# Kernel tuning notes

Hardware: AMD Instinct MI355X
Metric: run time of the kernel (lower is better)

The kernel has to match this reference:

```python
import jax, jax.numpy as jnp
import numpy as np

HIDDEN = 4096
NH = 32          # num query heads
NKV = 8          # num kv heads
HD = HIDDEN // NH  # 128
THETA = 10000.0
L = 4096         # llama_context_len (attention-sink window)
BS = 16          # paged KV block size
B = 16           # decode batch
MAXB = 385       # blocks per sequence
NBLOCKS = B * MAXB
CTX = 6145       # context_len for every sequence (num_past = 6144)


def rope(x, pos):
    """Neox-style RoPE. x: [..., H, HD]; pos: broadcastable to x.shape[:-2]."""
    half = HD // 2
    inv_freq = 1.0 / (THETA ** (jnp.arange(half, dtype=jnp.float32) * 2.0 / HD))
    ang = pos.astype(jnp.float32)[..., None] * inv_freq      # [..., half]
    cos = jnp.cos(ang)[..., None, :]                          # [..., 1, half]
    sin = jnp.sin(ang)[..., None, :]
    x1, x2 = x[..., :half], x[..., half:]
    return jnp.concatenate([x1 * cos - x2 * sin, x2 * cos + x1 * sin], axis=-1)


def setup_inputs() -> dict:
    key = jax.random.key(0)
    ks = jax.random.split(key, 6)
    hidden_states = jax.random.normal(ks[0], (B, HIDDEN), jnp.float32)
    positions = jax.random.randint(ks[1], (B,), 0, CTX).astype(jnp.int32)
    key_cache = jax.random.normal(ks[2], (NBLOCKS, NKV, HD, BS), jnp.float32)
    value_cache = jax.random.normal(ks[3], (NBLOCKS, NKV, HD, BS), jnp.float32)
    block_tables = jnp.arange(B * MAXB, dtype=jnp.int32).reshape(B, MAXB)
    w_qkv = jax.random.normal(ks[4], (HIDDEN, (NH + 2 * NKV) * HD), jnp.float32) * 0.02
    w_o = jax.random.normal(ks[5], (NH * HD, HIDDEN), jnp.float32) * 0.02
    return {
        "positions": positions,
        "hidden_states": hidden_states,
        "key_cache": key_cache,
        "value_cache": value_cache,
        "block_tables": block_tables,
        "context_len": CTX,
        "w_qkv": w_qkv,
        "w_o": w_o,
    }


def reference(positions, hidden_states, key_cache, value_cache, block_tables,
              context_len, w_qkv, w_o):
    # ---- qkv projection + split ----
    qkv = hidden_states @ w_qkv
    q, k, v = jnp.split(qkv, [NH * HD, NH * HD + NKV * HD], axis=-1)
    # ---- clamp positions to sink window and rope current q, k ----
    clamped = jnp.minimum(positions, L - 1)
    q = rope(q.reshape(B, NH, HD), clamped)          # [B, NH, HD]
    k = rope(k.reshape(B, NKV, HD), clamped)         # [B, NKV, HD]
    v = v.reshape(B, NKV, HD)

    # ---- static sink-window geometry (context_len is a Python int) ----
    num_past = context_len - 1
    blocks_to_ignore = (num_past - L) // BS + 1
    start = num_past - L + 1 + BS
    end = num_past

    # capped block table: token t<BS -> sink block bt[0];
    # t>=BS -> bt[blocks_to_ignore + t//BS]
    t = jnp.arange(L)
    logical = jnp.where(t < BS, 0, blocks_to_ignore + t // BS)   # [L]
    offset = t % BS                                              # [L]
    abs_pos = logical * BS + offset                              # [L] absolute position in seq

    phys = block_tables[:, logical]                              # [B, L]
    K = key_cache[phys, :, :, offset]                            # [B, L, NKV, HD]
    V = value_cache[phys, :, :, offset]

    # ---- sink RoPE rewrite: keys in [start, end) get an extra rotation at abs_pos-start ----
    rot_mask = (abs_pos >= start) & (abs_pos < end)
    K = jnp.where(rot_mask[None, :, None, None], rope(K, abs_pos - start), K)

    # ---- current token's freshly-rotated k/v occupy slot abs_pos == num_past ----
    cur = (abs_pos == num_past)
    K = jnp.where(cur[None, :, None, None], k[:, None, :, :], K)
    V = jnp.where(cur[None, :, None, None], v[:, None, :, :], V)

    # ---- GQA paged-decode attention over the 4096-token capped window ----
    valid = abs_pos <= num_past                                  # [L]
    G = NH // NKV
    qg = q.reshape(B, NKV, G, HD)
    scores = jnp.einsum('bkgd,blkd->bkgl', qg, K) * (HD ** -0.5)
    scores = jnp.where(valid[None, None, None, :], scores, jnp.finfo(scores.dtype).min)
    p = jax.nn.softmax(scores, axis=-1)
    attn = jnp.einsum('bkgl,blkd->bkgd', p, V).reshape(B, NH * HD)
    return attn @ w_o


if __name__ == "__main__":
    out = reference(**setup_inputs())
    print(out.shape, out.dtype)
```

## Files before the change

kernel.cpp:

```cpp
#include <hip/hip_runtime.h>
#include <math.h>

#define B_      16
#define NH      32
#define NKV     8
#define HD      128
#define GQ      4
#define LWIN    4096
#define BS      16
#define MAXB    385
#define HIDDEN  4096
#define QKV_COLS 6144
#define TAB_N   4100
#define T_CUR   4080
#define KS      64
#define NSPLIT  64
#define NCHUNK  8
#define SCALE   0.088388347648318447f
#define LOG1E4  9.210340371976184
#define TWO_PI  6.283185307179586
#define INV_2PI 0.15915494309189535

typedef float f4v __attribute__((ext_vector_type(4)));

__global__ void k_table(float* __restrict__ ctab, float* __restrict__ stab,
                        float* __restrict__ pk, float* __restrict__ pv) {
  int idx = blockIdx.x * 256 + threadIdx.x;
  if (idx < 64 * (TAB_N / 4)) {
    int d = idx / (TAB_N / 4);
    int q = idx - d * (TAB_N / 4);
    int i0 = q * 4;
    double f = exp(-(double)d / 64.0 * LOG1E4);
    double a = (double)(i0 - 1) * f;
    double rev = a * INV_2PI;
    rev -= rint(rev);
    float r = (float)(rev * TWO_PI);
    float c = cosf(r), s = sinf(r);
    float ff = (float)f;
    float cf = cosf(ff), sf = sinf(ff);
    int base = d * TAB_N + i0;
    ctab[base] = c; stab[base] = s;
#pragma unroll
    for (int j = 1; j < 4; j++) {
      float cn = c * cf - s * sf;
      float sn = s * cf + c * sf;
      c = cn; s = sn;
      ctab[base + j] = c; stab[base + j] = s;
    }
  }
  int nz = B_ * NKV * HD * BS;
  for (int z = idx; z < nz; z += gridDim.x * 256) { pk[z] = 0.f; pv[z] = 0.f; }
}

__global__ __launch_bounds__(128, 1) void k_gemm_part(
    const float* __restrict__ X, const float* __restrict__ W,
    float* __restrict__ part, int K, int ncols) {
  int tid = threadIdx.x;
  int k0 = blockIdx.y * KS;
  int n4 = (blockIdx.x * 128 + tid) * 4;
  f4v acc[B_];
#pragma unroll
  for (int b = 0; b < B_; b++) acc[b] = (f4v){0.f, 0.f, 0.f, 0.f};
  const float* wp = W + (size_t)k0 * ncols + n4;
  const float* xp = X + k0;
#pragma unroll
  for (int batch = 0; batch < KS / 16; batch++) {
    f4v w[16];
#pragma unroll
    for (int i = 0; i < 16; i++)
      w[i] = *(const f4v*)&wp[(size_t)(batch * 16 + i) * ncols];
#pragma unroll
    for (int i = 0; i < 16; i++) {
      int kk = batch * 16 + i;
#pragma unroll
      for (int b = 0; b < B_; b++) {
        float x = xp[b * K + kk];
        acc[b][0] = fmaf(x, w[i][0], acc[b][0]);
        acc[b][1] = fmaf(x, w[i][1], acc[b][1]);
        acc[b][2] = fmaf(x, w[i][2], acc[b][2]);
        acc[b][3] = fmaf(x, w[i][3], acc[b][3]);
      }
    }
  }
  float* pp = part + (size_t)blockIdx.y * B_ * ncols + n4;
#pragma unroll
  for (int b = 0; b < B_; b++) *(f4v*)&pp[(size_t)b * ncols] = acc[b];
}

__global__ __launch_bounds__(256) void k_qkv_finish(
    const float* __restrict__ part, const int* __restrict__ positions,
    const float* __restrict__ ctab, const float* __restrict__ stab,
    float* __restrict__ qout, float* __restrict__ pk, float* __restrict__ pv) {
  int idx = blockIdx.x * 256 + threadIdx.x;
  int b = idx / 3584;
  int u = idx - b * 3584;
  if (b >= B_) return;
  if (u < 2560) {
    int h = u >> 6, j = u & 63;
    int c1 = h * 128 + j;
    int c2 = c1 + 64;
    float s1 = 0.f, s2 = 0.f;
#pragma unroll 8
    for (int ky = 0; ky < NSPLIT; ky++) {
      const float* p = part + ((size_t)ky * B_ + b) * QKV_COLS;
      s1 += p[c1];
      s2 += p[c2];
    }
    int pos = min(positions[b], LWIN - 1);
    float c = ctab[j * TAB_N + pos + 1];
    float s = stab[j * TAB_N + pos + 1];
    float o1 = s1 * c - s2 * s;
    float o2 = s2 * c + s1 * s;
    if (h < NH) {
      qout[b * HIDDEN + c1] = o1;
      qout[b * HIDDEN + c2] = o2;
    } else {
      int kv = h - NH;
      pk[((b * NKV + kv) * HD + j) * BS] = o1;
      pk[((b * NKV + kv) * HD + j + 64) * BS] = o2;
    }
  } else {
    int vi = u - 2560;
    int kv = vi >> 7, d = vi & 127;
    int col = 5120 + vi;
    float s = 0.f;
#pragma unroll 8
    for (int ky = 0; ky < NSPLIT; ky++)
      s += part[((size_t)ky * B_ + b) * QKV_COLS + col];
    pv[((b * NKV + kv) * HD + d) * BS] = s;
  }
}

__global__ __launch_bounds__(128, 1) void k_attn(
    const float* __restrict__ kc, const float* __restrict__ vc,
    const int* __restrict__ bt, const float* __restrict__ qbuf,
    const float* __restrict__ pk, const float* __restrict__ pv,
    const float* __restrict__ ctab, const float* __restrict__ stab,
    float* __restrict__ partial) {
  __shared__ __align__(16) float qT[HD][GQ];
  __shared__ __align__(16) float p_s[512][GQ];
  __shared__ float redm[2][GQ];
  __shared__ float redl[2][GQ];
  __shared__ const float* kbase[32];
  __shared__ const float* vbase[32];

  int bx = blockIdx.x;
  int b = bx & 15, kv = bx >> 4;
  int chunk = blockIdx.y;
  int tid = threadIdx.x;
  int lane = tid & 63, wave = tid >> 6;

  for (int i = tid; i < GQ * HD; i += 128) {
    int g = i >> 7, d = i & 127;
    qT[d][g] = qbuf[b * HIDDEN + (kv * GQ + g) * HD + d];
  }
  if (tid < 32) {
    int tb = chunk * 32 + tid;
    if (tb == 255) {
      kbase[tid] = pk + (size_t)(b * NKV + kv) * (HD * BS);
      vbase[tid] = pv + (size_t)(b * NKV + kv) * (HD * BS);
    } else {
      int lg = (tb == 0) ? 0 : (129 + tb);
      size_t off = ((size_t)bt[b * MAXB + lg] * NKV + kv) * (HD * BS);
      kbase[tid] = kc + off;
      vbase[tid] = vc + off;
    }
  }
  __syncthreads();

  int blk_i = lane & 15, qq = lane >> 4;
  int t0 = chunk * 512 + wave * 256 + blk_i * 16 + qq * 4;
  const float* kb = kbase[wave * 16 + blk_i] + qq * 4;
  bool rot = (t0 >= 16) && (t0 < T_CUR);
  const float* ctp = ctab + t0;
  const float* stp = stab + t0;

  float sc[GQ][4];
#pragma unroll
  for (int g = 0; g < GQ; g++)
#pragma unroll
    for (int c = 0; c < 4; c++) sc[g][c] = 0.f;

#pragma unroll
  for (int batch = 0; batch < 8; batch++) {
    f4v k1[8], k2[8], cv[8], sv[8];
#pragma unroll
    for (int i = 0; i < 8; i++) {
      int d = batch * 8 + i;
      k1[i] = *(const f4v*)(kb + d * BS);
      k2[i] = *(const f4v*)(kb + (d + 64) * BS);
      cv[i] = *(const f4v*)(ctp + d * TAB_N);
      sv[i] = *(const f4v*)(stp + d * TAB_N);
    }
#pragma unroll
    for (int i = 0; i < 8; i++) {
      int d = batch * 8 + i;
      float4 q1 = *(const float4*)&qT[d][0];
      float4 q2 = *(const float4*)&qT[d + 64][0];
      float qg1[4] = {q1.x, q1.y, q1.z, q1.w};
      float qg2[4] = {q2.x, q2.y, q2.z, q2.w};
#pragma unroll
      for (int c = 0; c < 4; c++) {
        float cc = rot ? cv[i][c] : 1.f;
        float ss = rot ? sv[i][c] : 0.f;
        float r1 = k1[i][c] * cc - k2[i][c] * ss;
        float r2 = k2[i][c] * cc + k1[i][c] * ss;
#pragma unroll
        for (int g = 0; g < GQ; g++)
          sc[g][c] = fmaf(qg1[g], r1, fmaf(qg2[g], r2, sc[g][c]));
      }
    }
  }

  float mloc[GQ];
#pragma unroll
  for (int g = 0; g < GQ; g++) {
    float m = -3e38f;
#pragma unroll
    for (int c = 0; c < 4; c++) {
      float s = (t0 + c <= T_CUR) ? sc[g][c] * SCALE : -3e38f;
      sc[g][c] = s;
      m = fmaxf(m, s);
    }
#pragma unroll
    for (int off = 1; off < 64; off <<= 1) m = fmaxf(m, __shfl_xor(m, off, 64));
    mloc[g] = m;
  }
  if (lane == 0) {
#pragma unroll
    for (int g = 0; g < GQ; g++) redm[wave][g] = mloc[g];
  }
  __syncthreads();
  float mb[GQ];
#pragma unroll
  for (int g = 0; g < GQ; g++) mb[g] = fmaxf(redm[0][g], redm[1][g]);

  float4 prc[4];
  float ls[GQ] = {0.f, 0.f, 0.f, 0.f};
#pragma unroll
  for (int c = 0; c < 4; c++) {
    float p0 = __expf(sc[0][c] - mb[0]);
    float p1 = __expf(sc[1][c] - mb[1]);
    float p2 = __expf(sc[2][c] - mb[2]);
    float p3 = __expf(sc[3][c] - mb[3]);
    ls[0] += p0; ls[1] += p1; ls[2] += p2; ls[3] += p3;
    prc[c] = make_float4(p0, p1, p2, p3);
  }
#pragma unroll
  for (int g = 0; g < GQ; g++) {
    float v = ls[g];
#pragma unroll
    for (int off = 1; off < 64; off <<= 1) v += __shfl_xor(v, off, 64);
    ls[g] = v;
  }
  if (lane == 0) {
#pragma unroll
    for (int g = 0; g < GQ; g++) redl[wave][g] = ls[g];
  }
  int trow = t0 - chunk * 512;
#pragma unroll
  for (int c = 0; c < 4; c++) *(float4*)&p_s[trow + c][0] = prc[c];
  __syncthreads();

  float acc0 = 0.f, acc1 = 0.f, acc2 = 0.f, acc3 = 0.f;
  int d_own = tid;
#pragma unroll
  for (int bt4 = 0; bt4 < 8; bt4++) {
    f4v vr[4][4];
#pragma unroll
    for (int t = 0; t < 4; t++) {
      const float* vb = vbase[bt4 * 4 + t] + d_own * BS;
      vr[t][0] = *(const f4v*)(vb);
      vr[t][1] = *(const f4v*)(vb + 4);
      vr[t][2] = *(const f4v*)(vb + 8);
      vr[t][3] = *(const f4v*)(vb + 12);
    }
#pragma unroll
    for (int t = 0; t < 4; t++) {
      const float* pp = &p_s[(bt4 * 4 + t) * 16][0];
#pragma unroll
      for (int jq = 0; jq < 4; jq++) {
#pragma unroll
        for (int j = 0; j < 4; j++) {
          float4 pj = *(const float4*)(pp + (jq * 4 + j) * GQ);
          float vv = vr[t][jq][j];
          acc0 = fmaf(pj.x, vv, acc0);
          acc1 = fmaf(pj.y, vv, acc1);
          acc2 = fmaf(pj.z, vv, acc2);
          acc3 = fmaf(pj.w, vv, acc3);
        }
      }
    }
  }

  int pid = b * NKV + kv;
  float* pw = partial + ((size_t)pid * NCHUNK + chunk) * (GQ * 130);
  pw[0 * 130 + 2 + d_own] = acc0;
  pw[1 * 130 + 2 + d_own] = acc1;
  pw[2 * 130 + 2 + d_own] = acc2;
  pw[3 * 130 + 2 + d_own] = acc3;
  if (tid == 0) {
#pragma unroll
    for (int g = 0; g < GQ; g++) {
      pw[g * 130 + 0] = mb[g];
      pw[g * 130 + 1] = redl[0][g] + redl[1][g];
    }
  }
}

__global__ __launch_bounds__(512) void k_attn_combine(
    const float* __restrict__ partial, float* __restrict__ attn) {
  int pair = blockIdx.x;
  int tid = threadIdx.x;
  int g = tid >> 7, d = tid & 127;
  const float* pb = partial + (size_t)pair * NCHUNK * (GQ * 130) + g * 130;
  float M = -3e38f;
#pragma unroll
  for (int c = 0; c < NCHUNK; c++) M = fmaxf(M, pb[c * (GQ * 130)]);
  float L = 0.f, val = 0.f;
#pragma unroll
  for (int c = 0; c < NCHUNK; c++) {
    float m = pb[c * (GQ * 130)];
    float l = pb[c * (GQ * 130) + 1];
    float a = pb[c * (GQ * 130) + 2 + d];
    float w = __expf(m - M);
    L += l * w;
    val = fmaf(a, w, val);
  }
  int b = pair >> 3, kv = pair & 7;
  attn[b * HIDDEN + (kv * GQ + g) * HD + d] = val / L;
}

__global__ __launch_bounds__(256) void k_reduce_out(
    const float* __restrict__ part, float* __restrict__ out) {
  int idx = blockIdx.x * 256 + threadIdx.x;
  int b = idx >> 12, n = idx & 4095;
  float s = 0.f;
#pragma unroll 8
  for (int ky = 0; ky < NSPLIT; ky++)
    s += part[((size_t)ky * B_ + b) * HIDDEN + n];
  out[idx] = s;
}

extern "C" void kernel_launch(void* const* d_in, const int* in_sizes, int n_in,
                              void* d_out, int out_size, void* d_ws, size_t ws_size,
                              hipStream_t stream) {
  const int*   positions = (const int*)d_in[0];
  const float* hs        = (const float*)d_in[1];
  const float* kc        = (const float*)d_in[2];
  const float* vc        = (const float*)d_in[3];
  const int*   bt        = (const int*)d_in[4];
  const float* w_qkv     = (const float*)d_in[6];
  const float* w_o       = (const float*)d_in[7];
  float* out = (float*)d_out;

  float* ws    = (float*)d_ws;
  float* ctab  = ws;
  float* stab  = ctab + 262400;
  float* pk    = stab + 262400;
  float* pv    = pk + 262144;
  float* qbuf  = pv + 262144;
  float* apart = qbuf + 65536;
  float* attn  = apart + 532480;
  float* gpart = attn + 65536;

  k_table<<<257, 256, 0, stream>>>(ctab, stab, pk, pv);
  k_gemm_part<<<dim3(QKV_COLS / 512, NSPLIT), 128, 0, stream>>>(hs, w_qkv, gpart, HIDDEN, QKV_COLS);
  k_qkv_finish<<<(B_ * 3584) / 256, 256, 0, stream>>>(gpart, positions, ctab, stab, qbuf, pk, pv);
  k_attn<<<dim3(B_ * NKV, NCHUNK), 128, 0, stream>>>(kc, vc, bt, qbuf, pk, pv, ctab, stab, apart);
  k_attn_combine<<<B_ * NKV, 512, 0, stream>>>(apart, attn);
  k_gemm_part<<<dim3(HIDDEN / 512, NSPLIT), 128, 0, stream>>>(attn, w_o, gpart, HIDDEN, HIDDEN);
  k_reduce_out<<<(B_ * HIDDEN) / 256, 256, 0, stream>>>(gpart, out);
}
```

Baseline: 216.7 us.

## Restructure QK loop for coalesced per-block K loads with cross-lane reduction

Rewrites the QK score loop so each wave processes one paged KV block at a time, with lanes splitting the head dimension. The K and RoPE table loads become contiguous across lanes, and the partial dot products are combined with xor shuffles and staged through shared memory before the softmax. This aims to replace the previously strided per-lane K reads with coalesced ones. It also changes the split configuration (KS 128, NSPLIT 32), which adds shuffle and sync overhead and changes the launch shape.

Result: slower. 252.0 us (+16.3%).

```diff
diff --git a/kernel.cpp b/kernel.cpp
--- a/kernel.cpp
+++ b/kernel.cpp
@@ -13,8 +13,8 @@
 #define QKV_COLS 6144
 #define TAB_N   4100
 #define T_CUR   4080
-#define KS      64
-#define NSPLIT  64
+#define KS      128
+#define NSPLIT  32
 #define NCHUNK  8
 #define SCALE   0.088388347648318447f
 #define LOG1E4  9.210340371976184
@@ -168,33 +168,36 @@
   }
   __syncthreads();
 
-  int blk_i = lane & 15, qq = lane >> 4;
-  int t0 = chunk * 512 + wave * 256 + blk_i * 16 + qq * 4;
-  const float* kb = kbase[wave * 16 + blk_i] + qq * 4;
-  bool rot = (t0 >= 16) && (t0 < T_CUR);
-  const float* ctp = ctab + t0;
-  const float* stp = stab + t0;
-
-  float sc[GQ][4];
-#pragma unroll
-  for (int g = 0; g < GQ; g++)
-#pragma unroll
-    for (int c = 0; c < 4; c++) sc[g][c] = 0.f;
-
-#pragma unroll
-  for (int batch = 0; batch < 8; batch++) {
-    f4v k1[8], k2[8], cv[8], sv[8];
-#pragma unroll
-    for (int i = 0; i < 8; i++) {
-      int d = batch * 8 + i;
-      k1[i] = *(const f4v*)(kb + d * BS);
-      k2[i] = *(const f4v*)(kb + (d + 64) * BS);
-      cv[i] = *(const f4v*)(ctp + d * TAB_N);
-      sv[i] = *(const f4v*)(stp + d * TAB_N);
-    }
-#pragma unroll
-    for (int i = 0; i < 8; i++) {
-      int d = batch * 8 + i;
+  int dl = lane >> 2;
+  int q  = lane & 3;
+#pragma unroll 2
+  for (int j = 0; j < 16; j++) {
+    int jj = wave * 16 + j;
+    const float* kb = kbase[jj];
+    int tg = chunk * 512 + jj * 16 + q * 4;
+    bool rot = (tg >= 16) && (tg < T_CUR);
+
+    f4v k[8];
+#pragma unroll
+    for (int i = 0; i < 8; i++)
+      k[i] = *(const f4v*)(kb + i * 256 + dl * 16 + q * 4);
+    f4v cv[4], sv[4];
+#pragma unroll
+    for (int i = 0; i < 4; i++) {
+      int d = i * 16 + dl;
+      cv[i] = *(const f4v*)(ctab + (size_t)d * TAB_N + tg);
+      sv[i] = *(const f4v*)(stab + (size_t)d * TAB_N + tg);
+    }
+
+    float sc[GQ][4];
+#pragma unroll
+    for (int g = 0; g < GQ; g++)
+#pragma unroll
+      for (int c = 0; c < 4; c++) sc[g][c] = 0.f;
+
+#pragma unroll
+    for (int i = 0; i < 4; i++) {
+      int d = i * 16 + dl;
       float4 q1 = *(const float4*)&qT[d][0];
       float4 q2 = *(const float4*)&qT[d + 64][0];
       float qg1[4] = {q1.x, q1.y, q1.z, q1.w};
@@ -203,15 +206,43 @@
       for (int c = 0; c < 4; c++) {
         float cc = rot ? cv[i][c] : 1.f;
         float ss = rot ? sv[i][c] : 0.f;
-        float r1 = k1[i][c] * cc - k2[i][c] * ss;
-        float r2 = k2[i][c] * cc + k1[i][c] * ss;
+        float r1 = k[i][c] * cc - k[i + 4][c] * ss;
+        float r2 = k[i + 4][c] * cc + k[i][c] * ss;
 #pragma unroll
         for (int g = 0; g < GQ; g++)
           sc[g][c] = fmaf(qg1[g], r1, fmaf(qg2[g], r2, sc[g][c]));
       }
     }
-  }
-
+
+#pragma unroll
+    for (int g = 0; g < GQ; g++)
+#pragma unroll
+      for (int c = 0; c < 4; c++) {
+        float v = sc[g][c];
+        v += __shfl_xor(v, 4, 64);
+        v += __shfl_xor(v, 8, 64);
+        v += __shfl_xor(v, 16, 64);
+        v += __shfl_xor(v, 32, 64);
+        sc[g][c] = v;
+      }
+    if (dl == 0) {
+#pragma unroll
+      for (int c = 0; c < 4; c++)
+        *(float4*)&p_s[jj * 16 + q * 4 + c][0] =
+            make_float4(sc[0][c], sc[1][c], sc[2][c], sc[3][c]);
+    }
+  }
+  __syncthreads();
+
+  int blk_i = lane & 15, qq = lane >> 4;
+  int trow = wave * 256 + blk_i * 16 + qq * 4;
+  int t0 = chunk * 512 + trow;
+  float sc[GQ][4];
+#pragma unroll
+  for (int c = 0; c < 4; c++) {
+    float4 r = *(const float4*)&p_s[trow + c][0];
+    sc[0][c] = r.x; sc[1][c] = r.y; sc[2][c] = r.z; sc[3][c] = r.w;
+  }
   float mloc[GQ];
 #pragma unroll
   for (int g = 0; g < GQ; g++) {
@@ -257,7 +288,6 @@
 #pragma unroll
     for (int g = 0; g < GQ; g++) redl[wave][g] = ls[g];
   }
-  int trow = t0 - chunk * 512;
 #pragma unroll
   for (int c = 0; c < 4; c++) *(float4*)&p_s[trow + c][0] = prc[c];
   __syncthreads();
```
